# Performance work log

Hardware: AMD Instinct MI355X
Metric: run time of the kernel (lower is better)

## Reference

```python
import jax, jax.numpy as jnp
import numpy as np

B = 65536   # batch (number of parallel envs)
HID = 64    # GRU hidden / FC width
ACT = 3     # action count


def setup_inputs() -> dict:
    key = jax.random.key(0)
    ks = iter(jax.random.split(key, 64))

    def rn(shape, s=0.1):
        return jax.random.normal(next(ks), shape, dtype=jnp.float32) * s

    inp = {
        "obs": jax.random.uniform(next(ks), (B, 7, 7, 3), dtype=jnp.float32, maxval=10.0),
        "memory": rn((B, 4 * HID), 1.0),
        "conv_w1": rn((16, 3, 2, 2)), "conv_b1": rn((16,)),
        "conv_w2": rn((32, 16, 2, 2)), "conv_b2": rn((32,)),
        "conv_w3": rn((64, 32, 2, 2)), "conv_b3": rn((64,)),
    }
    for g in ("g1", "g2"):
        for l in (0, 1):
            inp[f"{g}_wih{l}"] = rn((3 * HID, HID))
            inp[f"{g}_whh{l}"] = rn((3 * HID, HID))
            inp[f"{g}_bih{l}"] = rn((3 * HID,))
            inp[f"{g}_bhh{l}"] = rn((3 * HID,))
    inp.update({
        "actor_w1": rn((HID, HID)), "actor_b1": rn((HID,)),
        "actor_w2": rn((ACT, HID)), "actor_b2": rn((ACT,)),
        "critic_w1": rn((HID, HID)), "critic_b1": rn((HID,)),
        "critic_w2": rn((1, HID)), "critic_b2": rn((1,)),
    })
    return inp


def _conv(x, w, b):
    # NCHW, OIHW, VALID, stride 1 (matches nn.Conv2d defaults)
    y = jax.lax.conv_general_dilated(x, w, (1, 1), 'VALID',
                                     dimension_numbers=('NCHW', 'OIHW', 'NCHW'))
    return y + b[None, :, None, None]


def _maxpool2(x):
    return jax.lax.reduce_window(x, -jnp.inf, jax.lax.max,
                                 (1, 1, 2, 2), (1, 1, 2, 2), 'VALID')


def _gru_cell(x, h, wih, whh, bih, bhh):
    # PyTorch GRU cell math (gate order: r, z, n)
    gi = x @ wih.T + bih
    gh = h @ whh.T + bhh
    i_r, i_z, i_n = jnp.split(gi, 3, axis=-1)
    h_r, h_z, h_n = jnp.split(gh, 3, axis=-1)
    r = jax.nn.sigmoid(i_r + h_r)
    z = jax.nn.sigmoid(i_z + h_z)
    n = jnp.tanh(i_n + r * h_n)
    return (1.0 - z) * n + z * h


def reference(obs, memory, conv_w1, conv_b1, conv_w2, conv_b2, conv_w3, conv_b3,
              g1_wih0, g1_whh0, g1_bih0, g1_bhh0, g1_wih1, g1_whh1, g1_bih1, g1_bhh1,
              g2_wih0, g2_whh0, g2_bih0, g2_bhh0, g2_wih1, g2_whh1, g2_bih1, g2_bhh1,
              actor_w1, actor_b1, actor_w2, actor_b2,
              critic_w1, critic_b1, critic_w2, critic_b2):
    bsz = memory.shape[0]
    # obs.transpose(1,3).transpose(2,3): NHWC -> NCHW
    x = jnp.transpose(obs, (0, 3, 1, 2))
    x = jax.nn.relu(_conv(x, conv_w1, conv_b1))   # [B,16,6,6]
    x = _maxpool2(x)                              # [B,16,3,3]
    x = jax.nn.relu(_conv(x, conv_w2, conv_b2))   # [B,32,2,2]
    x = jax.nn.relu(_conv(x, conv_w3, conv_b3))   # [B,64,1,1]
    x = x.reshape(bsz, -1)                        # [B,64]

    h1 = memory[:, :2 * HID].reshape(bsz, 2, HID)
    h2 = memory[:, 2 * HID:].reshape(bsz, 2, HID)

    # single-timestep 2-layer GRU #1
    inp = x
    h1_new = []
    for l, (wih, whh, bih, bhh) in enumerate([(g1_wih0, g1_whh0, g1_bih0, g1_bhh0),
                                              (g1_wih1, g1_whh1, g1_bih1, g1_bhh1)]):
        inp = _gru_cell(inp, h1[:, l], wih, whh, bih, bhh)
        h1_new.append(inp)
    mem1 = jnp.stack(h1_new, axis=1).reshape(bsz, 2 * HID)

    # single-timestep 2-layer GRU #2 (input = GRU1 top-layer output)
    h2_new = []
    for l, (wih, whh, bih, bhh) in enumerate([(g2_wih0, g2_whh0, g2_bih0, g2_bhh0),
                                              (g2_wih1, g2_whh1, g2_bih1, g2_bhh1)]):
        inp = _gru_cell(inp, h2[:, l], wih, whh, bih, bhh)
        h2_new.append(inp)
    mem2 = jnp.stack(h2_new, axis=1).reshape(bsz, 2 * HID)

    embedding = inp  # GRU2 top-layer output, [B,64]

    logits = jax.nn.relu(embedding @ actor_w1.T + actor_b1) @ actor_w2.T + actor_b2
    log_probs = jax.nn.log_softmax(logits, axis=1)          # Categorical(logits=log_softmax)
    value = (jax.nn.relu(embedding @ critic_w1.T + critic_b1) @ critic_w2.T + critic_b2)[:, 0]
    memory_out = jnp.concatenate([mem1, mem2], axis=1)      # [B,256]
    return (log_probs, value, memory_out)
```

## Files before the change

### kernel.cpp

```cpp
#include <hip/hip_runtime.h>

#define BATCH 65536
#define NT 256
#define NTG 512
#define MFMA __builtin_amdgcn_mfma_f32_16x16x32_bf16

typedef short bf16x8 __attribute__((ext_vector_type(8)));
typedef float f32x4 __attribute__((ext_vector_type(4)));
typedef unsigned short u16x8 __attribute__((ext_vector_type(8)));

__device__ __forceinline__ float sigmoidf_(float x) { return 1.0f / (1.0f + __expf(-x)); }
__device__ __forceinline__ float tanhf_(float x) { return 2.0f / (1.0f + __expf(-2.0f * x)) - 1.0f; }
__device__ __forceinline__ unsigned short f2b(float f) {
  union { float f; unsigned int u; } v; v.f = f;
  unsigned int r = (v.u + 0x7FFFu + ((v.u >> 16) & 1u)) >> 16;
  return (unsigned short)r;
}
__device__ __forceinline__ float b2f(unsigned short u) {
  return __uint_as_float(((unsigned int)u) << 16);
}
__device__ __forceinline__ bf16x8 cvt8(float4 a, float4 b) {
  union { unsigned short u[8]; bf16x8 v; } t;
  t.u[0] = f2b(a.x); t.u[1] = f2b(a.y); t.u[2] = f2b(a.z); t.u[3] = f2b(a.w);
  t.u[4] = f2b(b.x); t.u[5] = f2b(b.y); t.u[6] = f2b(b.z); t.u[7] = f2b(b.w);
  return t.v;
}

__global__ __launch_bounds__(NT) void k_prep(
    const float* __restrict__ W0, const float* __restrict__ W1,
    const float* __restrict__ W2, const float* __restrict__ W3,
    const float* __restrict__ W4, const float* __restrict__ W5,
    const float* __restrict__ W6, const float* __restrict__ W7,
    const float* __restrict__ bi0, const float* __restrict__ bi1,
    const float* __restrict__ bi2, const float* __restrict__ bi3,
    const float* __restrict__ bh0, const float* __restrict__ bh1,
    const float* __restrict__ bh2, const float* __restrict__ bh3,
    const float* __restrict__ aw1, const float* __restrict__ cw1,
    const float* __restrict__ w3s,
    unsigned short* __restrict__ wsW, unsigned short* __restrict__ wsH,
    unsigned short* __restrict__ wsW3, float* __restrict__ wsB) {
  const int y = blockIdx.y;
  const int i = blockIdx.x * NT + threadIdx.x;
  if (y < 8) {
    if (i >= 12288) return;
    const float* src = (y == 0) ? W0 : (y == 1) ? W1 : (y == 2) ? W2 : (y == 3) ? W3
                     : (y == 4) ? W4 : (y == 5) ? W5 : (y == 6) ? W6 : W7;
    const int c = y >> 1, p = y & 1;
    const int j = i >> 6, k = i & 63;
    const int g = j >> 6, jrow = j & 63;
    const int jt = jrow >> 4, r16i = jrow & 15;
    const int kseg = k >> 5, kgv = (k & 31) >> 3, e = k & 7;
    const int lane = kgv * 16 + r16i;
    const int q = g * 4 + p * 2 + kseg;
    wsW[c * 24576 + ((jt * 12 + q) * 64 + lane) * 8 + e] = f2b(src[i]);
  } else if (y == 8) {
    if (i < 4096) wsH[i] = f2b(aw1[i]);
  } else if (y == 9) {
    if (i < 4096) wsH[4096 + i] = f2b(cw1[i]);
  } else if (y == 10) {
    if (i < 8192) wsW3[i] = f2b(w3s[i]);
  } else {
    const int c = y - 11;
    if (i < 256) {
      const float* bi = (c == 0) ? bi0 : (c == 1) ? bi1 : (c == 2) ? bi2 : bi3;
      const float* bh = (c == 0) ? bh0 : (c == 1) ? bh1 : (c == 2) ? bh2 : bh3;
      const int j = i & 63, g = i >> 6;
      float v = (g == 0) ? bi[j] + bh[j]
              : (g == 1) ? bi[64 + j] + bh[64 + j]
              : (g == 2) ? bi[128 + j] : bh[128 + j];
      wsB[c * 256 + i] = v;
    }
  }
}

#define OSTR 149
#define PSTR 146
__global__ __launch_bounds__(NT) void k_conv12(const float* __restrict__ obs,
                                               const float* __restrict__ w1,
                                               const float* __restrict__ b1,
                                               const float* __restrict__ w2,
                                               const float* __restrict__ b2,
                                               unsigned short* __restrict__ c2b) {
  __shared__ float obs_f[64 * OSTR];
  __shared__ unsigned short pooled[64 * PSTR];
  const int tid = threadIdx.x;
  const int lane = tid & 63;
  const int wave = tid >> 6;
  const int m_base = blockIdx.x * 64;

  {
    const float4* src = (const float4*)(obs + (size_t)m_base * 147);
#pragma unroll 1
    for (int i = tid; i < 2352; i += NT) {
      const float4 v = src[i];
      int idx = i * 4;
      int s = idx / 147;
      int c = idx - s * 147;
      obs_f[s * OSTR + c] = v.x;
      if (++c == 147) { c = 0; ++s; } obs_f[s * OSTR + c] = v.y;
      if (++c == 147) { c = 0; ++s; } obs_f[s * OSTR + c] = v.z;
      if (++c == 147) { c = 0; ++s; } obs_f[s * OSTR + c] = v.w;
    }
  }
  __syncthreads();

  if (wave < 3) {
    const int ph = wave, s = lane;
    float r[3][21];
#pragma unroll
    for (int rr = 0; rr < 3; ++rr)
#pragma unroll
      for (int i = 0; i < 21; ++i) r[rr][i] = obs_f[s * OSTR + (2 * ph + rr) * 21 + i];
#pragma unroll 1
    for (int oc = 0; oc < 16; ++oc) {
      float wv[12];
#pragma unroll
      for (int i = 0; i < 12; ++i) wv[i] = w1[oc * 12 + i];
      const float bias = b1[oc];
#pragma unroll
      for (int pw = 0; pw < 3; ++pw) {
        float m = 0.0f;
#pragma unroll
        for (int dh = 0; dh < 2; ++dh)
#pragma unroll
          for (int dw = 0; dw < 2; ++dw) {
            float acc = bias;
#pragma unroll
            for (int kh = 0; kh < 2; ++kh)
#pragma unroll
              for (int kw = 0; kw < 2; ++kw)
#pragma unroll
                for (int c = 0; c < 3; ++c)
                  acc += r[dh + kh][(2 * pw + dw + kw) * 3 + c] * wv[c * 4 + kh * 2 + kw];
            m = fmaxf(m, fmaxf(acc, 0.0f));
          }
        pooled[s * PSTR + oc * 9 + ph * 3 + pw] = f2b(m);
      }
    }
  }
  __syncthreads();

  {
    const int g = wave, s = lane;
    const int ocb = g * 8;
    float acc[8][4];
#pragma unroll
    for (int u = 0; u < 8; ++u) {
      const float bb = b2[ocb + u];
      acc[u][0] = bb; acc[u][1] = bb; acc[u][2] = bb; acc[u][3] = bb;
    }
#pragma unroll 1
    for (int ic = 0; ic < 16; ++ic) {
      float p9[9];
#pragma unroll
      for (int p = 0; p < 9; ++p) p9[p] = b2f(pooled[s * PSTR + ic * 9 + p]);
#pragma unroll
      for (int u = 0; u < 8; ++u) {
        float w[4];
#pragma unroll
        for (int i = 0; i < 4; ++i) w[i] = w2[((ocb + u) * 16 + ic) * 4 + i];
#pragma unroll
        for (int oh = 0; oh < 2; ++oh)
#pragma unroll
          for (int ow = 0; ow < 2; ++ow)
            acc[u][oh * 2 + ow] += p9[(oh + 0) * 3 + (ow + 0)] * w[0] +
                                   p9[(oh + 0) * 3 + (ow + 1)] * w[1] +
                                   p9[(oh + 1) * 3 + (ow + 0)] * w[2] +
                                   p9[(oh + 1) * 3 + (ow + 1)] * w[3];
      }
    }
    unsigned short ob[32];
#pragma unroll
    for (int u = 0; u < 8; ++u)
#pragma unroll
      for (int p = 0; p < 4; ++p) ob[u * 4 + p] = f2b(fmaxf(acc[u][p], 0.0f));
#pragma unroll
    for (int i = 0; i < 4; ++i)
      *(u16x8*)(c2b + (size_t)(m_base + s) * 128 + g * 32 + 8 * i) = *(const u16x8*)(ob + 8 * i);
  }
}

#define XSTR 88
__global__ __launch_bounds__(NTG, 4) void k_gru(
    const unsigned short* __restrict__ c2b,
    const float* __restrict__ memF,
    const unsigned short* __restrict__ wsW,
    const unsigned short* __restrict__ wsW3,
    const float* __restrict__ wsB,
    const unsigned short* __restrict__ wsH,
    const float* __restrict__ b3,
    const float* __restrict__ ab1, const float* __restrict__ cb1,
    const float* __restrict__ aw2, const float* __restrict__ ab2,
    const float* __restrict__ cw2, const float* __restrict__ cb2,
    float* __restrict__ out) {
  __shared__ unsigned short wlds[24576];
  __shared__ unsigned short xls[128 * XSTR];
  const int tid = threadIdx.x;
  const int lane = tid & 63;
  const int wave = tid >> 6;
  const int r16 = lane & 15;
  const int kg = lane >> 4;
  const int wbase = wave * 16;
  const int m_base = blockIdx.x * 128 + wbase;
  float* outMem = out + (size_t)4 * BATCH;

  float4 wst[6];
  {
    const float4* wsrc = (const float4*)wsW;
#pragma unroll
    for (int r = 0; r < 6; ++r) wst[r] = wsrc[r * NTG + tid];
  }
  bf16x8 a0[4];
  {
    const unsigned short* ap = c2b + (size_t)(m_base + r16) * 128 + kg * 8;
#pragma unroll
    for (int f = 0; f < 4; ++f) a0[f] = *(const bf16x8*)(ap + f * 32);
  }
  float4 hraw[4];
  {
    const float* hp = memF + (size_t)(m_base + r16) * 256 + kg * 8;
    hraw[0] = *(const float4*)(hp);
    hraw[1] = *(const float4*)(hp + 4);
    hraw[2] = *(const float4*)(hp + 32);
    hraw[3] = *(const float4*)(hp + 36);
  }

#pragma unroll
  for (int n = 0; n < 4; ++n) {
    const float bias = b3[n * 16 + r16];
    const unsigned short* bp = wsW3 + (size_t)(n * 16 + r16) * 128 + kg * 8;
    f32x4 q0 = (f32x4)(0.0f);
#pragma unroll
    for (int f = 0; f < 4; ++f) {
      bf16x8 b = *(const bf16x8*)(bp + f * 32);
      q0 = MFMA(a0[f], b, q0, 0, 0, 0);
    }
#pragma unroll
    for (int q = 0; q < 4; ++q)
      xls[(wbase + kg * 4 + q) * XSTR + n * 16 + r16] = f2b(fmaxf(q0[q] + bias, 0.0f));
  }
  {
    float4* wd = (float4*)wlds;
#pragma unroll
    for (int r = 0; r < 6; ++r) wd[r * NTG + tid] = wst[r];
  }
  __syncthreads();

#pragma unroll 1
  for (int c = 0; c < 4; ++c) {
    const int co = c * 64;
    const float* bcp = wsB + c * 256;
    bf16x8 ax0, ax1, ah0, ah1;
    {
      const unsigned short* xp = xls + (wbase + r16) * XSTR + kg * 8;
      ax0 = *(const bf16x8*)(xp);
      ax1 = *(const bf16x8*)(xp + 32);
    }
    ah0 = cvt8(make_float4(hraw[0].x, hraw[0].y, hraw[0].z, hraw[0].w),
               make_float4(hraw[1].x, hraw[1].y, hraw[1].z, hraw[1].w));
    ah1 = cvt8(make_float4(hraw[2].x, hraw[2].y, hraw[2].z, hraw[2].w),
               make_float4(hraw[3].x, hraw[3].y, hraw[3].z, hraw[3].w));
    if (c < 3) {
      const float* hp = memF + (size_t)(m_base + r16) * 256 + (c + 1) * 64 + kg * 8;
      hraw[0] = *(const float4*)(hp);
      hraw[1] = *(const float4*)(hp + 4);
      hraw[2] = *(const float4*)(hp + 32);
      hraw[3] = *(const float4*)(hp + 36);
    }
    const unsigned short* wl = wlds + lane * 8;
#pragma unroll 2
    for (int jt = 0; jt < 4; ++jt) {
      const unsigned short* wjt = wl + jt * 6144;
      bf16x8 xr0 = *(const bf16x8*)(wjt);
      bf16x8 xr1 = *(const bf16x8*)(wjt + 512);
      bf16x8 hr0 = *(const bf16x8*)(wjt + 1024);
      bf16x8 hr1 = *(const bf16x8*)(wjt + 1536);
      bf16x8 xz0 = *(const bf16x8*)(wjt + 2048);
      bf16x8 xz1 = *(const bf16x8*)(wjt + 2560);
      bf16x8 hz0 = *(const bf16x8*)(wjt + 3072);
      bf16x8 hz1 = *(const bf16x8*)(wjt + 3584);
      bf16x8 xn0 = *(const bf16x8*)(wjt + 4096);
      bf16x8 xn1 = *(const bf16x8*)(wjt + 4608);
      bf16x8 hn0 = *(const bf16x8*)(wjt + 5120);
      bf16x8 hn1 = *(const bf16x8*)(wjt + 5632);
      f32x4 sr = (f32x4)(0.0f), sz = (f32x4)(0.0f), sn = (f32x4)(0.0f), tn = (f32x4)(0.0f);
      sr = MFMA(ax0, xr0, sr, 0, 0, 0);
      sr = MFMA(ax1, xr1, sr, 0, 0, 0);
      sr = MFMA(ah0, hr0, sr, 0, 0, 0);
      sr = MFMA(ah1, hr1, sr, 0, 0, 0);
      sz = MFMA(ax0, xz0, sz, 0, 0, 0);
      sz = MFMA(ax1, xz1, sz, 0, 0, 0);
      sz = MFMA(ah0, hz0, sz, 0, 0, 0);
      sz = MFMA(ah1, hz1, sz, 0, 0, 0);
      sn = MFMA(ax0, xn0, sn, 0, 0, 0);
      sn = MFMA(ax1, xn1, sn, 0, 0, 0);
      tn = MFMA(ah0, hn0, tn, 0, 0, 0);
      tn = MFMA(ah1, hn1, tn, 0, 0, 0);
      float ho[4];
      {
        const size_t base = (size_t)(m_base + kg * 4) * 256 + co + jt * 16 + r16;
        ho[0] = memF[base];       ho[1] = memF[base + 256];
        ho[2] = memF[base + 512]; ho[3] = memF[base + 768];
      }
      const float rb = bcp[jt * 16 + r16];
      const float zb = bcp[64 + jt * 16 + r16];
      const float inb = bcp[128 + jt * 16 + r16];
      const float hnb = bcp[192 + jt * 16 + r16];
#pragma unroll
      for (int q = 0; q < 4; ++q) {
        const int sq = m_base + kg * 4 + q;
        const float rg = sigmoidf_(sr[q] + rb);
        const float zg = sigmoidf_(sz[q] + zb);
        const float ng = tanhf_((sn[q] + inb) + rg * (tn[q] + hnb));
        const float nh = (1.0f - zg) * ng + zg * ho[q];
        outMem[(size_t)sq * 256 + co + jt * 16 + r16] = nh;
        xls[(wbase + kg * 4 + q) * XSTR + jt * 16 + r16] = f2b(nh);
      }
    }
    if (c < 3) {
      __syncthreads();
      const float4* wsrc = (const float4*)(wsW + (size_t)(c + 1) * 24576);
      float4* wd = (float4*)wlds;
#pragma unroll
      for (int r = 0; r < 6; ++r) wd[r * NTG + tid] = wsrc[r * NTG + tid];
      __syncthreads();
    }
  }

  bf16x8 ex0, ex1;
  {
    const unsigned short* xp = xls + (wbase + r16) * XSTR + kg * 8;
    ex0 = *(const bf16x8*)(xp);
    ex1 = *(const bf16x8*)(xp + 32);
  }
  f32x4 ha[8];
#pragma unroll
  for (int n = 0; n < 8; ++n) ha[n] = (f32x4)(0.0f);
#pragma unroll
  for (int n = 0; n < 8; ++n) {
    const unsigned short* wp = wsH + (size_t)(n * 16 + r16) * 64 + kg * 8;
    bf16x8 b0 = *(const bf16x8*)(wp);
    bf16x8 b1 = *(const bf16x8*)(wp + 32);
    ha[n] = MFMA(ex0, b0, ha[n], 0, 0, 0);
    ha[n] = MFMA(ex1, b1, ha[n], 0, 0, 0);
  }
  float w2a0[4], w2a1[4], w2a2[4], w2cc[4], bav[4], bcv[4];
#pragma unroll
  for (int t = 0; t < 4; ++t) {
    const int j = 16 * t + r16;
    w2a0[t] = aw2[j]; w2a1[t] = aw2[64 + j]; w2a2[t] = aw2[128 + j];
    w2cc[t] = cw2[j]; bav[t] = ab1[j]; bcv[t] = cb1[j];
  }
  const float b20 = ab2[0], b21 = ab2[1], b22 = ab2[2], b2c = cb2[0];
#pragma unroll
  for (int q = 0; q < 4; ++q) {
    float l0 = 0.0f, l1 = 0.0f, l2 = 0.0f, vv = 0.0f;
#pragma unroll
    for (int t = 0; t < 4; ++t) {
      const float av = fmaxf(ha[t][q] + bav[t], 0.0f);
      const float cv = fmaxf(ha[t + 4][q] + bcv[t], 0.0f);
      l0 += av * w2a0[t]; l1 += av * w2a1[t]; l2 += av * w2a2[t];
      vv += cv * w2cc[t];
    }
#pragma unroll
    for (int m = 1; m < 16; m <<= 1) {
      l0 += __shfl_xor(l0, m); l1 += __shfl_xor(l1, m);
      l2 += __shfl_xor(l2, m); vv += __shfl_xor(vv, m);
    }
    if (r16 == 0) {
      const int sq = m_base + kg * 4 + q;
      const float g0 = l0 + b20, g1 = l1 + b21, g2 = l2 + b22;
      const float mx = fmaxf(g0, fmaxf(g1, g2));
      const float lse = mx + __logf(__expf(g0 - mx) + __expf(g1 - mx) + __expf(g2 - mx));
      out[(size_t)sq * 3 + 0] = g0 - lse;
      out[(size_t)sq * 3 + 1] = g1 - lse;
      out[(size_t)sq * 3 + 2] = g2 - lse;
      out[(size_t)3 * BATCH + sq] = vv + b2c;
    }
  }
}

extern "C" void kernel_launch(void* const* d_in, const int* in_sizes, int n_in,
                              void* d_out, int out_size, void* d_ws, size_t ws_size,
                              hipStream_t stream) {
  (void)in_sizes; (void)n_in; (void)out_size; (void)ws_size;
  const float* obs = (const float*)d_in[0];
  const float* mem = (const float*)d_in[1];
  const float* w1 = (const float*)d_in[2];
  const float* b1 = (const float*)d_in[3];
  const float* w2 = (const float*)d_in[4];
  const float* b2 = (const float*)d_in[5];
  const float* w3 = (const float*)d_in[6];
  const float* b3 = (const float*)d_in[7];
  const float* gw[16];
  for (int i = 0; i < 16; ++i) gw[i] = (const float*)d_in[8 + i];
  const float* aw1 = (const float*)d_in[24];
  const float* ab1 = (const float*)d_in[25];
  const float* aw2 = (const float*)d_in[26];
  const float* ab2 = (const float*)d_in[27];
  const float* cw1 = (const float*)d_in[28];
  const float* cb1 = (const float*)d_in[29];
  const float* cw2 = (const float*)d_in[30];
  const float* cb2 = (const float*)d_in[31];

  float* out = (float*)d_out;

  unsigned short* c2b = (unsigned short*)d_ws;
  unsigned short* wsW = c2b + (size_t)128 * BATCH;
  unsigned short* wsH = wsW + 98304;
  unsigned short* wsW3 = wsH + 8192;
  float* wsB = (float*)(wsW3 + 8192);

  const dim3 blk(NT);
  hipLaunchKernelGGL(k_prep, dim3(48, 15), blk, 0, stream,
                     gw[0], gw[1], gw[4], gw[5], gw[8], gw[9], gw[12], gw[13],
                     gw[2], gw[6], gw[10], gw[14],
                     gw[3], gw[7], gw[11], gw[15],
                     aw1, cw1, w3, wsW, wsH, wsW3, wsB);
  hipLaunchKernelGGL(k_conv12, dim3(BATCH / 64), blk, 0, stream,
                     obs, w1, b1, w2, b2, c2b);
  hipLaunchKernelGGL(k_gru, dim3(BATCH / 128), dim3(NTG), 0, stream,
                     c2b, mem, wsW, wsW3, wsB, wsH, b3,
                     ab1, cb1, aw2, ab2, cw2, cb2, out);
}
```

Baseline: 110.0 us.

## Swap MFMA operand order so each lane owns a row for vectorized stores

After: 112.2 us. No clear change (+2.0%).

```diff
diff --git a/kernel.cpp b/kernel.cpp
--- a/kernel.cpp
+++ b/kernel.cpp
@@ -8,6 +8,7 @@
 typedef short bf16x8 __attribute__((ext_vector_type(8)));
 typedef float f32x4 __attribute__((ext_vector_type(4)));
 typedef unsigned short u16x8 __attribute__((ext_vector_type(8)));
+typedef unsigned short u16x4 __attribute__((ext_vector_type(4)));
 
 __device__ __forceinline__ float sigmoidf_(float x) { return 1.0f / (1.0f + __expf(-x)); }
 __device__ __forceinline__ float tanhf_(float x) { return 2.0f / (1.0f + __expf(-2.0f * x)) - 1.0f; }
@@ -227,17 +228,18 @@
 
 #pragma unroll
   for (int n = 0; n < 4; ++n) {
-    const float bias = b3[n * 16 + r16];
     const unsigned short* bp = wsW3 + (size_t)(n * 16 + r16) * 128 + kg * 8;
     f32x4 q0 = (f32x4)(0.0f);
 #pragma unroll
     for (int f = 0; f < 4; ++f) {
       bf16x8 b = *(const bf16x8*)(bp + f * 32);
-      q0 = MFMA(a0[f], b, q0, 0, 0, 0);
-    }
-#pragma unroll
-    for (int q = 0; q < 4; ++q)
-      xls[(wbase + kg * 4 + q) * XSTR + n * 16 + r16] = f2b(fmaxf(q0[q] + bias, 0.0f));
+      q0 = MFMA(b, a0[f], q0, 0, 0, 0);
+    }
+    const f32x4 b4 = *(const f32x4*)(b3 + n * 16 + kg * 4);
+    u16x4 xo;
+#pragma unroll
+    for (int q = 0; q < 4; ++q) xo[q] = f2b(fmaxf(q0[q] + b4[q], 0.0f));
+    *(u16x4*)(xls + (wbase + r16) * XSTR + n * 16 + kg * 4) = xo;
   }
   {
     float4* wd = (float4*)wlds;
@@ -268,7 +270,7 @@
       hraw[3] = *(const float4*)(hp + 36);
     }
     const unsigned short* wl = wlds + lane * 8;
-#pragma unroll 2
+#pragma unroll 1
     for (int jt = 0; jt < 4; ++jt) {
       const unsigned short* wjt = wl + jt * 6144;
       bf16x8 xr0 = *(const bf16x8*)(wjt);
@@ -284,38 +286,37 @@
       bf16x8 hn0 = *(const bf16x8*)(wjt + 5120);
       bf16x8 hn1 = *(const bf16x8*)(wjt + 5632);
       f32x4 sr = (f32x4)(0.0f), sz = (f32x4)(0.0f), sn = (f32x4)(0.0f), tn = (f32x4)(0.0f);
-      sr = MFMA(ax0, xr0, sr, 0, 0, 0);
-      sr = MFMA(ax1, xr1, sr, 0, 0, 0);
-      sr = MFMA(ah0, hr0, sr, 0, 0, 0);
-      sr = MFMA(ah1, hr1, sr, 0, 0, 0);
-      sz = MFMA(ax0, xz0, sz, 0, 0, 0);
-      sz = MFMA(ax1, xz1, sz, 0, 0, 0);
-      sz = MFMA(ah0, hz0, sz, 0, 0, 0);
-      sz = MFMA(ah1, hz1, sz, 0, 0, 0);
-      sn = MFMA(ax0, xn0, sn, 0, 0, 0);
-      sn = MFMA(ax1, xn1, sn, 0, 0, 0);
-      tn = MFMA(ah0, hn0, tn, 0, 0, 0);
-      tn = MFMA(ah1, hn1, tn, 0, 0, 0);
-      float ho[4];
-      {
-        const size_t base = (size_t)(m_base + kg * 4) * 256 + co + jt * 16 + r16;
-        ho[0] = memF[base];       ho[1] = memF[base + 256];
-        ho[2] = memF[base + 512]; ho[3] = memF[base + 768];
+      sr = MFMA(xr0, ax0, sr, 0, 0, 0);
+      sr = MFMA(xr1, ax1, sr, 0, 0, 0);
+      sr = MFMA(hr0, ah0, sr, 0, 0, 0);
+      sr = MFMA(hr1, ah1, sr, 0, 0, 0);
+      sz = MFMA(xz0, ax0, sz, 0, 0, 0);
+      sz = MFMA(xz1, ax1, sz, 0, 0, 0);
+      sz = MFMA(hz0, ah0, sz, 0, 0, 0);
+      sz = MFMA(hz1, ah1, sz, 0, 0, 0);
+      sn = MFMA(xn0, ax0, sn, 0, 0, 0);
+      sn = MFMA(xn1, ax1, sn, 0, 0, 0);
+      tn = MFMA(hn0, ah0, tn, 0, 0, 0);
+      tn = MFMA(hn1, ah1, tn, 0, 0, 0);
+      const int jb = jt * 16 + kg * 4;
+      const f32x4 ho4 = *(const f32x4*)(memF + (size_t)(m_base + r16) * 256 + co + jb);
+      const f32x4 rb4 = *(const f32x4*)(bcp + jb);
+      const f32x4 zb4 = *(const f32x4*)(bcp + 64 + jb);
+      const f32x4 ib4 = *(const f32x4*)(bcp + 128 + jb);
+      const f32x4 hb4 = *(const f32x4*)(bcp + 192 + jb);
+      f32x4 nhv;
+      u16x4 xo;
+#pragma unroll
+      for (int q = 0; q < 4; ++q) {
+        const float rg = sigmoidf_(sr[q] + rb4[q]);
+        const float zg = sigmoidf_(sz[q] + zb4[q]);
+        const float ng = tanhf_((sn[q] + ib4[q]) + rg * (tn[q] + hb4[q]));
+        const float nh = (1.0f - zg) * ng + zg * ho4[q];
+        nhv[q] = nh;
+        xo[q] = f2b(nh);
       }
-      const float rb = bcp[jt * 16 + r16];
-      const float zb = bcp[64 + jt * 16 + r16];
-      const float inb = bcp[128 + jt * 16 + r16];
-      const float hnb = bcp[192 + jt * 16 + r16];
-#pragma unroll
-      for (int q = 0; q < 4; ++q) {
-        const int sq = m_base + kg * 4 + q;
-        const float rg = sigmoidf_(sr[q] + rb);
-        const float zg = sigmoidf_(sz[q] + zb);
-        const float ng = tanhf_((sn[q] + inb) + rg * (tn[q] + hnb));
-        const float nh = (1.0f - zg) * ng + zg * ho[q];
-        outMem[(size_t)sq * 256 + co + jt * 16 + r16] = nh;
-        xls[(wbase + kg * 4 + q) * XSTR + jt * 16 + r16] = f2b(nh);
-      }
+      *(f32x4*)(outMem + (size_t)(m_base + r16) * 256 + co + jb) = nhv;
+      *(u16x4*)(xls + (wbase + r16) * XSTR + jb) = xo;
     }
     if (c < 3) {
       __syncthreads();
@@ -341,42 +342,40 @@
     const unsigned short* wp = wsH + (size_t)(n * 16 + r16) * 64 + kg * 8;
     bf16x8 b0 = *(const bf16x8*)(wp);
     bf16x8 b1 = *(const bf16x8*)(wp + 32);
-    ha[n] = MFMA(ex0, b0, ha[n], 0, 0, 0);
-    ha[n] = MFMA(ex1, b1, ha[n], 0, 0, 0);
-  }
-  float w2a0[4], w2a1[4], w2a2[4], w2cc[4], bav[4], bcv[4];
+    ha[n] = MFMA(b0, ex0, ha[n], 0, 0, 0);
+    ha[n] = MFMA(b1, ex1, ha[n], 0, 0, 0);
+  }
+  float l0 = 0.0f, l1 = 0.0f, l2 = 0.0f, vv = 0.0f;
+  const int jb0 = kg * 4;
 #pragma unroll
   for (int t = 0; t < 4; ++t) {
-    const int j = 16 * t + r16;
-    w2a0[t] = aw2[j]; w2a1[t] = aw2[64 + j]; w2a2[t] = aw2[128 + j];
-    w2cc[t] = cw2[j]; bav[t] = ab1[j]; bcv[t] = cb1[j];
-  }
-  const float b20 = ab2[0], b21 = ab2[1], b22 = ab2[2], b2c = cb2[0];
-#pragma unroll
-  for (int q = 0; q < 4; ++q) {
-    float l0 = 0.0f, l1 = 0.0f, l2 = 0.0f, vv = 0.0f;
-#pragma unroll
-    for (int t = 0; t < 4; ++t) {
-      const float av = fmaxf(ha[t][q] + bav[t], 0.0f);
-      const float cv = fmaxf(ha[t + 4][q] + bcv[t], 0.0f);
-      l0 += av * w2a0[t]; l1 += av * w2a1[t]; l2 += av * w2a2[t];
-      vv += cv * w2cc[t];
-    }
-#pragma unroll
-    for (int m = 1; m < 16; m <<= 1) {
-      l0 += __shfl_xor(l0, m); l1 += __shfl_xor(l1, m);
-      l2 += __shfl_xor(l2, m); vv += __shfl_xor(vv, m);
-    }
-    if (r16 == 0) {
-      const int sq = m_base + kg * 4 + q;
-      const float g0 = l0 + b20, g1 = l1 + b21, g2 = l2 + b22;
-      const float mx = fmaxf(g0, fmaxf(g1, g2));
-      const float lse = mx + __logf(__expf(g0 - mx) + __expf(g1 - mx) + __expf(g2 - mx));
-      out[(size_t)sq * 3 + 0] = g0 - lse;
-      out[(size_t)sq * 3 + 1] = g1 - lse;
-      out[(size_t)sq * 3 + 2] = g2 - lse;
-      out[(size_t)3 * BATCH + sq] = vv + b2c;
-    }
+    const f32x4 ba4 = *(const f32x4*)(ab1 + t * 16 + jb0);
+    const f32x4 w0 = *(const f32x4*)(aw2 + t * 16 + jb0);
+    const f32x4 w1 = *(const f32x4*)(aw2 + 64 + t * 16 + jb0);
+    const f32x4 w2v = *(const f32x4*)(aw2 + 128 + t * 16 + jb0);
+    const f32x4 bc4 = *(const f32x4*)(cb1 + t * 16 + jb0);
+    const f32x4 wc4 = *(const f32x4*)(cw2 + t * 16 + jb0);
+#pragma unroll
+    for (int q = 0; q < 4; ++q) {
+      const float av = fmaxf(ha[t][q] + ba4[q], 0.0f);
+      const float cv = fmaxf(ha[t + 4][q] + bc4[q], 0.0f);
+      l0 += av * w0[q]; l1 += av * w1[q]; l2 += av * w2v[q];
+      vv += cv * wc4[q];
+    }
+  }
+  l0 += __shfl_xor(l0, 16); l0 += __shfl_xor(l0, 32);
+  l1 += __shfl_xor(l1, 16); l1 += __shfl_xor(l1, 32);
+  l2 += __shfl_xor(l2, 16); l2 += __shfl_xor(l2, 32);
+  vv += __shfl_xor(vv, 16); vv += __shfl_xor(vv, 32);
+  if (kg == 0) {
+    const int sq = m_base + r16;
+    const float g0 = l0 + ab2[0], g1 = l1 + ab2[1], g2 = l2 + ab2[2];
+    const float mx = fmaxf(g0, fmaxf(g1, g2));
+    const float lse = mx + __logf(__expf(g0 - mx) + __expf(g1 - mx) + __expf(g2 - mx));
+    out[(size_t)sq * 3 + 0] = g0 - lse;
+    out[(size_t)sq * 3 + 1] = g1 - lse;
+    out[(size_t)sq * 3 + 2] = g2 - lse;
+    out[(size_t)3 * BATCH + sq] = vv + cb2[0];
   }
 }
 
```
